# Performance work log

Hardware: AMD Instinct MI355X
Metric: run time of the kernel (lower is better)

The kernel has to match this reference:

```python
import jax, jax.numpy as jnp
import numpy as np

B, CIN, COUT, N, T, K = 16, 32, 64, 1024, 64, 3


def setup_inputs() -> dict:
    key = jax.random.key(0)
    k1, k2, k3 = jax.random.split(key, 3)
    x = jax.random.normal(k1, (B, CIN, N, T), dtype=jnp.float32)
    # scaled laplacian-like support (keep spectral radius ~1 so Chebyshev terms stay bounded)
    adj = jax.random.normal(k2, (N, N), dtype=jnp.float32) / np.sqrt(N).astype(np.float32)
    W = jax.random.normal(k3, (4 * COUT, (CIN + COUT) * K), dtype=jnp.float32) * 0.02
    b = jnp.zeros((4 * COUT,), dtype=jnp.float32)
    return {"x": x, "adj": adj, "W": W, "b": b}


def reference(x, adj, W, b):
    Bn, cin, Nn, Tn = x.shape
    c_out = W.shape[0] // 4
    feat_in = W.shape[1] // K  # = cin + c_out

    # Chebyshev polynomial basis of adj (loop-invariant across time; compute once)
    Ls = [jnp.eye(Nn, dtype=x.dtype), adj]
    for _ in range(2, K):
        Ls.append(2.0 * (adj @ Ls[-1]) - Ls[-2])
    Lap = jnp.stack(Ls, 0)  # [K, N, N]; Ls[k][q, n]

    # Conv1d(kernel=1) weight reshaped to match channel flatten order (c major, k minor)
    Wr = W.reshape(4 * c_out, feat_in, K)  # [4*c_out, F, K]
    bb = b[None, :, None]

    def step(carry, xt):
        h, c = carry
        tem = jnp.concatenate([xt, h], axis=1)  # [B, F, N]
        # einsum('bcn,knq->bckq', x, Lap.T) == einsum('bfn,kqn->bfkq', x, Lap)
        g = jnp.einsum('bfn,kqn->bfkq', tem, Lap)  # [B, F, K, N]
        fea = jnp.einsum('bfkq,ofk->boq', g, Wr) + bb  # [B, 4*c_out, N]
        i, j, f, o = jnp.split(fea, 4, axis=1)
        new_c = c * jax.nn.sigmoid(f) + jax.nn.sigmoid(i) * jnp.tanh(j)
        new_h = jnp.tanh(new_c) * jax.nn.sigmoid(o)
        return (new_h, new_c), new_h

    h0 = jnp.zeros((Bn, c_out, Nn), dtype=x.dtype)
    c0 = jnp.zeros((Bn, c_out, Nn), dtype=x.dtype)
    x_t = jnp.moveaxis(x, -1, 0)  # [T, B, cin, N]
    _, outs = jax.lax.scan(step, (h0, c0), x_t)  # [T, B, c_out, N]
    return jnp.moveaxis(outs, 0, -1)  # [B, c_out, N, T]
```

## Files before the change

### kernel.cpp

```cpp
#include <hip/hip_runtime.h>
#include <stdint.h>


#define Bb   16
#define CIN  32
#define COUT 64
#define Nn   1024
#define Tt   64
#define Ff   96
#define G4   256
#define KJ   288

#define BUFSZ 40960
#define GQPB  624
#define GQLO  19968
#define SCP   100

typedef unsigned short u16;
typedef short short8 __attribute__((ext_vector_type(8)));
typedef short short4v __attribute__((ext_vector_type(4)));
typedef float f32x4 __attribute__((ext_vector_type(4)));

static __device__ __forceinline__ u16 f2bf(float f) {
    union { float f; uint32_t u; } v; v.f = f;
    uint32_t r = v.u + 0x7FFFu + ((v.u >> 16) & 1u);
    return (u16)(r >> 16);
}
static __device__ __forceinline__ float bf2f(u16 h) {
    union { uint32_t u; float f; } v; v.u = ((uint32_t)h) << 16;
    return v.f;
}
static __device__ __forceinline__ float sigm(float x) { return 1.0f / (1.0f + expf(-x)); }

static __device__ __forceinline__ void gload16(const void* g, void* l) {
    __builtin_amdgcn_global_load_lds(
        (const __attribute__((address_space(1))) void*)g,
        (__attribute__((address_space(3))) void*)l, 16, 0, 0);
}

__global__ void k_fill(float* out, int n, float v) {
    int i = blockIdx.x * 256 + threadIdx.x;
    if (i < n) out[i] = v;
}

__global__ __launch_bounds__(256) void k_adj_split(const float* __restrict__ adj,
                                                   u16* __restrict__ hi, u16* __restrict__ lo) {
    int i = blockIdx.x * 256 + threadIdx.x;
    float v = adj[i];
    u16 h = f2bf(v);
    hi[i] = h; lo[i] = f2bf(v - bf2f(h));
}

__global__ __launch_bounds__(256) void k_adj_t(const float* __restrict__ adj,
                                               u16* __restrict__ th, u16* __restrict__ tl_) {
    __shared__ float tile[64][65];
    int m0 = blockIdx.x * 64, n0 = blockIdx.y * 64;
    int tid = threadIdx.x;
    #pragma unroll
    for (int i = 0; i < 16; i++) {
        int lin = i * 256 + tid;
        int ml = lin >> 6, nl = lin & 63;
        tile[ml][nl] = adj[(size_t)(m0 + ml) * Nn + n0 + nl];
    }
    __syncthreads();
    #pragma unroll
    for (int i = 0; i < 16; i++) {
        int lin = i * 256 + tid;
        int nl = lin >> 6, ml = lin & 63;
        float v = tile[ml][nl];
        u16 h = f2bf(v);
        size_t off = (size_t)(n0 + nl) * Nn + m0 + ml;
        th[off] = h; tl_[off] = f2bf(v - bf2f(h));
    }
}

__global__ __launch_bounds__(256) void k_l2(
    const u16* __restrict__ a_hi, const u16* __restrict__ a_lo,
    const u16* __restrict__ bt_hi, const u16* __restrict__ bt_lo,
    u16* __restrict__ o_hi, u16* __restrict__ o_lo)
{
    __shared__ u16 Ah[64][40], Al[64][40], Bh[64][40], Bl[64][40];
    const int tid = threadIdx.x, lane = tid & 63, w = tid >> 6;
    const int wm = (w >> 1) * 32, wn = (w & 1) * 32;
    const int r0 = blockIdx.x * 64, q0 = blockIdx.y * 64;
    const int srow = tid >> 2, scol = (tid & 3) * 8;
    const u16* arh = a_hi + (size_t)(r0 + srow) * Nn;
    const u16* arl = a_lo + (size_t)(r0 + srow) * Nn;
    const u16* brh = bt_hi + (size_t)(q0 + srow) * Nn;
    const u16* brl = bt_lo + (size_t)(q0 + srow) * Nn;

    f32x4 acc[2][2];
    #pragma unroll
    for (int i = 0; i < 2; i++)
        #pragma unroll
        for (int j = 0; j < 2; j++) acc[i][j] = (f32x4){0.f, 0.f, 0.f, 0.f};

    for (int k0 = 0; k0 < Nn; k0 += 32) {
        __syncthreads();
        *(short8*)&Ah[srow][scol] = *(const short8*)&arh[k0 + scol];
        *(short8*)&Al[srow][scol] = *(const short8*)&arl[k0 + scol];
        *(short8*)&Bh[srow][scol] = *(const short8*)&brh[k0 + scol];
        *(short8*)&Bl[srow][scol] = *(const short8*)&brl[k0 + scol];
        __syncthreads();
        const int kb = (lane >> 4) * 8;
        short8 ah[2], al[2], bh[2], bl[2];
        #pragma unroll
        for (int mi = 0; mi < 2; mi++) {
            int row = wm + mi * 16 + (lane & 15);
            ah[mi] = *(const short8*)&Ah[row][kb];
            al[mi] = *(const short8*)&Al[row][kb];
        }
        #pragma unroll
        for (int ni = 0; ni < 2; ni++) {
            int col = wn + ni * 16 + (lane & 15);
            bh[ni] = *(const short8*)&Bh[col][kb];
            bl[ni] = *(const short8*)&Bl[col][kb];
        }
        #pragma unroll
        for (int mi = 0; mi < 2; mi++)
            #pragma unroll
            for (int ni = 0; ni < 2; ni++) {
                acc[mi][ni] = __builtin_amdgcn_mfma_f32_16x16x32_bf16(ah[mi], bh[ni], acc[mi][ni], 0, 0, 0);
                acc[mi][ni] = __builtin_amdgcn_mfma_f32_16x16x32_bf16(al[mi], bh[ni], acc[mi][ni], 0, 0, 0);
                acc[mi][ni] = __builtin_amdgcn_mfma_f32_16x16x32_bf16(ah[mi], bl[ni], acc[mi][ni], 0, 0, 0);
            }
    }
    #pragma unroll
    for (int mi = 0; mi < 2; mi++)
        #pragma unroll
        for (int ni = 0; ni < 2; ni++)
            #pragma unroll
            for (int j = 0; j < 4; j++) {
                int rr = r0 + wm + mi * 16 + (lane >> 4) * 4 + j;
                int qq = q0 + wn + ni * 16 + (lane & 15);
                float v = 2.f * acc[mi][ni][j] - ((rr == qq) ? 1.f : 0.f);
                size_t off = (size_t)rr * Nn + qq;
                u16 hh = f2bf(v);
                o_hi[off] = hh; o_lo[off] = f2bf(v - bf2f(hh));
            }
}

__global__ __launch_bounds__(256) void k_w_split(const float* __restrict__ W,
                                                 u16* __restrict__ hi, u16* __restrict__ lo) {
    int idx = blockIdx.x * 256 + threadIdx.x;
    int o = idx / KJ, j = idx - o * KJ;
    int k = j / Ff, f = j - k * Ff;
    float v = W[(size_t)o * KJ + f * 3 + k];
    u16 h = f2bf(v);
    hi[idx] = h; lo[idx] = f2bf(v - bf2f(h));
}

__global__ __launch_bounds__(256) void k_x_split(const float* __restrict__ x,
        u16* __restrict__ xf_hi, u16* __restrict__ xf_lo) {
    __shared__ float tile[64][65];
    int n0 = blockIdx.x * 64;
    int bc = blockIdx.y;
    const float* src = x + (size_t)bc * Nn * Tt;
    int tid = threadIdx.x;
    #pragma unroll
    for (int i = 0; i < 16; i++) {
        int lin = i * 256 + tid;
        int nl = lin >> 6, tl = lin & 63;
        tile[nl][tl] = src[(size_t)(n0 + nl) * Tt + tl];
    }
    __syncthreads();
    int b = bc >> 5, ch = bc & 31;
    #pragma unroll
    for (int i = 0; i < 2; i++) {
        int item = i * 256 + tid;
        int tl = item >> 3, oct = item & 7;
        short8 vh, vl;
        #pragma unroll
        for (int m = 0; m < 8; m++) {
            float v = tile[oct * 8 + m][tl];
            u16 h = f2bf(v);
            vh[m] = (short)h;
            vl[m] = (short)f2bf(v - bf2f(h));
        }
        size_t off = (((size_t)tl * Bb + b) * CIN + ch) * Nn + n0 + oct * 8;
        *(short8*)&xf_hi[off] = vh;
        *(short8*)&xf_lo[off] = vl;
    }
}

__global__ __launch_bounds__(512, 4) void k_step(
    int t,
    const u16* __restrict__ xsf_hi, const u16* __restrict__ xsf_lo,
    u16* __restrict__ hf_hi, u16* __restrict__ hf_lo,
    const u16* __restrict__ bcat_hi, const u16* __restrict__ bcat_lo,
    const u16* __restrict__ Wh, const u16* __restrict__ Wl,
    const float* __restrict__ bias, float* __restrict__ cbuf,
    float* __restrict__ outbuf)
{
    __shared__ __attribute__((aligned(16))) char lds[81920];
    const int tid = threadIdx.x, lane = tid & 63, w = tid >> 6;
    const int bx = blockIdx.x;
    const int q0g = bx * 32;
    const int bb = blockIdx.y;

    const u16* srcb[5];
    #pragma unroll
    for (int i = 0; i < 5; i++) {
        int u = i * 512 + tid;
        if (u < 1536) {
            int hl = (u >= 768) ? 1 : 0;
            int r = (u - hl * 768) >> 3, c8 = u & 7;
            const u16* p;
            if (r < CIN) p = (hl ? xsf_lo : xsf_hi) + (size_t)((t * Bb + bb) * CIN + r) * Nn;
            else         p = (hl ? hf_lo  : hf_hi ) + (size_t)(bb * COUT + r - CIN) * Nn;
            srcb[i] = p + (c8 ^ (r & 7)) * 8;
        } else {
            int v = u - 1536;
            int hl = v >> 9;
            int r = (v & 511) >> 3, c8 = v & 7;
            int grow = q0g + (r & 31) + ((r >= 32) ? Nn : 0);
            srcb[i] = (hl ? bcat_lo : bcat_hi) + (size_t)grow * Nn + (c8 ^ (r & 7)) * 8;
        }
    }

    const int kg = w >> 2;
    const int wsub = w & 3;
    const int wr = wsub >> 1, wc = wsub & 1;
    const int ksw = kg * 4 + (lane >> 4);

    f32x4 acc[3][2];
    #pragma unroll
    for (int i = 0; i < 3; i++)
        #pragma unroll
        for (int j = 0; j < 2; j++) acc[i][j] = (f32x4){0.f, 0.f, 0.f, 0.f};

    u16 cxh[6], cxl[6];
    #pragma unroll
    for (int i = 0; i < 6; i++) { cxh[i] = 0; cxl[i] = 0; }
    const int capkc = bx >> 1;

    #pragma unroll
    for (int i = 0; i < 5; i++)
        gload16(srcb[i], lds + (i * 512 + tid) * 16);

    for (int kc = 0; kc < 16; kc++) {
        if (kc < 15) {
            char* nb = lds + ((kc + 1) & 1) * BUFSZ;
            const int k0 = (kc + 1) * 64;
            #pragma unroll
            for (int i = 0; i < 5; i++)
                gload16(srcb[i] + k0, nb + (i * 512 + tid) * 16);
            asm volatile("s_waitcnt vmcnt(5)" ::: "memory");
        } else {
            asm volatile("s_waitcnt vmcnt(0)" ::: "memory");
        }
        __builtin_amdgcn_s_barrier();
        const char* bo = lds + (kc & 1) * BUFSZ;
        {
            short8 ah[3], al[3], bh[2], bl[2];
            #pragma unroll
            for (int mi = 0; mi < 3; mi++) {
                int r = wr * 48 + mi * 16 + (lane & 15);
                int off = r * 128 + ((ksw ^ (r & 7)) << 4);
                ah[mi] = *(const short8*)(bo + off);
                al[mi] = *(const short8*)(bo + 12288 + off);
            }
            #pragma unroll
            for (int ni = 0; ni < 2; ni++) {
                int rb = wc * 32 + ni * 16 + (lane & 15);
                int off = 24576 + rb * 128 + ((ksw ^ (rb & 7)) << 4);
                bh[ni] = *(const short8*)(bo + off);
                bl[ni] = *(const short8*)(bo + 8192 + off);
            }
            __builtin_amdgcn_s_setprio(1);
            #pragma unroll
            for (int mi = 0; mi < 3; mi++)
                #pragma unroll
                for (int ni = 0; ni < 2; ni++) {
                    acc[mi][ni] = __builtin_amdgcn_mfma_f32_16x16x32_bf16(ah[mi], bh[ni], acc[mi][ni], 0, 0, 0);
                    acc[mi][ni] = __builtin_amdgcn_mfma_f32_16x16x32_bf16(al[mi], bh[ni], acc[mi][ni], 0, 0, 0);
                    acc[mi][ni] = __builtin_amdgcn_mfma_f32_16x16x32_bf16(ah[mi], bl[ni], acc[mi][ni], 0, 0, 0);
                }
            __builtin_amdgcn_s_setprio(0);
        }
        if (kc == capkc) {
            int q = lane & 31;
            int jg = (w << 1) | (lane >> 5);
            int lc = ((bx & 1) << 5) | q;
            int u8 = lc >> 3, byoff = (lc & 7) * 2;
            #pragma unroll
            for (int jj = 0; jj < 6; jj++) {
                int j = jg * 6 + jj;
                int off = j * 128 + (((u8) ^ (j & 7)) << 4) + byoff;
                cxh[jj] = *(const u16*)(bo + off);
                cxl[jj] = *(const u16*)(bo + 12288 + off);
            }
            asm volatile("s_waitcnt lgkmcnt(0)" ::: "memory");
            __builtin_amdgcn_sched_barrier(0);
        }
        __builtin_amdgcn_s_barrier();
    }

    {
        float* scratch = (float*)(lds + BUFSZ);
        if (kg == 0) {
            #pragma unroll
            for (int mi = 0; mi < 3; mi++)
                #pragma unroll
                for (int ni = 0; ni < 2; ni++) {
                    int c = wc * 32 + ni * 16 + (lane & 15);
                    int r0 = wr * 48 + mi * 16 + (lane >> 4) * 4;
                    *(f32x4*)&scratch[c * SCP + r0] = acc[mi][ni];
                }
        }
        __syncthreads();
        if (kg == 1) {
            #pragma unroll
            for (int mi = 0; mi < 3; mi++)
                #pragma unroll
                for (int ni = 0; ni < 2; ni++) {
                    int c = wc * 32 + ni * 16 + (lane & 15);
                    int r0 = wr * 48 + mi * 16 + (lane >> 4) * 4;
                    acc[mi][ni] += *(const f32x4*)&scratch[c * SCP + r0];
                }
        }
    }

    {
        int q = lane & 31;
        int jg = (w << 1) | (lane >> 5);
        #pragma unroll
        for (int jj = 0; jj < 6; jj++) {
            int j = jg * 6 + jj;
            *(u16*)(lds + q * GQPB + j * 2) = cxh[jj];
            *(u16*)(lds + GQLO + q * GQPB + j * 2) = cxl[jj];
        }
    }
    if (kg == 1) {
        #pragma unroll
        for (int mi = 0; mi < 3; mi++)
            #pragma unroll
            for (int ni = 0; ni < 2; ni++) {
                int c = wc * 32 + ni * 16 + (lane & 15);
                int g = c >> 5, ql = c & 31;
                int f0 = wr * 48 + mi * 16 + (lane >> 4) * 4;
                int jd = 96 + g * 96 + f0;
                short4v vh, vl;
                #pragma unroll
                for (int j = 0; j < 4; j++) {
                    float v = acc[mi][ni][j];
                    u16 hh = f2bf(v);
                    vh[j] = (short)hh;
                    vl[j] = (short)f2bf(v - bf2f(hh));
                }
                *(short4v*)(lds + ql * GQPB + jd * 2) = vh;
                *(short4v*)(lds + GQLO + ql * GQPB + jd * 2) = vl;
            }
    }
    __syncthreads();

    f32x4 a2[2][2];
    #pragma unroll
    for (int i = 0; i < 2; i++)
        #pragma unroll
        for (int j = 0; j < 2; j++) a2[i][j] = (f32x4){0.f, 0.f, 0.f, 0.f};

    const int kb8 = (lane >> 4) * 8;
    #pragma unroll
    for (int c = 0; c < 9; c++) {
        int j0 = c * 32;
        short8 wh[2], wl2[2], gh[2], gl[2];
        #pragma unroll
        for (int mi = 0; mi < 2; mi++) {
            int o = w * 32 + mi * 16 + (lane & 15);
            size_t so = (size_t)o * KJ + j0 + kb8;
            wh[mi]  = *(const short8*)&Wh[so];
            wl2[mi] = *(const short8*)&Wl[so];
        }
        #pragma unroll
        for (int ni = 0; ni < 2; ni++) {
            int q = ni * 16 + (lane & 15);
            int off = q * GQPB + (j0 + kb8) * 2;
            gh[ni] = *(const short8*)(lds + off);
            gl[ni] = *(const short8*)(lds + GQLO + off);
        }
        #pragma unroll
        for (int mi = 0; mi < 2; mi++)
            #pragma unroll
            for (int ni = 0; ni < 2; ni++) {
                a2[mi][ni] = __builtin_amdgcn_mfma_f32_16x16x32_bf16(wh[mi],  gh[ni], a2[mi][ni], 0, 0, 0);
                a2[mi][ni] = __builtin_amdgcn_mfma_f32_16x16x32_bf16(wl2[mi], gh[ni], a2[mi][ni], 0, 0, 0);
                a2[mi][ni] = __builtin_amdgcn_mfma_f32_16x16x32_bf16(wh[mi],  gl[ni], a2[mi][ni], 0, 0, 0);
            }
    }
    __syncthreads();

    {
        float* FEAf = (float*)lds;
        #pragma unroll
        for (int mi = 0; mi < 2; mi++) {
            int o0 = w * 32 + mi * 16 + (lane >> 4) * 4;
            f32x4 bv = *(const f32x4*)&bias[o0];
            #pragma unroll
            for (int ni = 0; ni < 2; ni++) {
                int q = ni * 16 + (lane & 15);
                #pragma unroll
                for (int j = 0; j < 4; j++)
                    FEAf[(o0 + j) * 33 + q] = a2[mi][ni][j] + bv[j];
            }
        }
    }
    __syncthreads();

    {
        const float* FEAf = (const float*)lds;
        int q = tid & 31, qg = q0g + q;
        int co0 = (tid >> 5) * 4;
        #pragma unroll
        for (int ii = 0; ii < 4; ii++) {
            int co = co0 + ii;
            float iv = FEAf[co * 33 + q];
            float jv = FEAf[(co + 64) * 33 + q];
            float fv = FEAf[(co + 128) * 33 + q];
            float ov = FEAf[(co + 192) * 33 + q];
            size_t cof = ((size_t)(bb * COUT + co)) * Nn + qg;
            float cc = cbuf[cof];
            float nc = cc * sigm(fv) + sigm(iv) * tanhf(jv);
            float nh = tanhf(nc) * sigm(ov);
            cbuf[cof] = nc;
            u16 hh = f2bf(nh);
            hf_hi[cof] = hh; hf_lo[cof] = f2bf(nh - bf2f(hh));
            outbuf[((size_t)(t * Bb + bb) * COUT + co) * Nn + qg] = nh;
        }
    }
}

__global__ __launch_bounds__(256) void k_out_t(const float* __restrict__ outbuf,
                                               float* __restrict__ out) {
    __shared__ float tile[64][65];
    int q0 = blockIdx.x * 64;
    int bo = blockIdx.y;
    int b = bo >> 6, o = bo & 63;
    int tid = threadIdx.x;
    #pragma unroll
    for (int i = 0; i < 16; i++) {
        int lin = i * 256 + tid;
        int tl = lin >> 6, ql = lin & 63;
        tile[tl][ql] = outbuf[(((size_t)tl * Bb + b) * COUT + o) * Nn + q0 + ql];
    }
    __syncthreads();
    #pragma unroll
    for (int i = 0; i < 16; i++) {
        int lin = i * 256 + tid;
        int ql = lin >> 6, tl = lin & 63;
        out[((size_t)bo * Nn + q0 + ql) * Tt + tl] = tile[tl][ql];
    }
}

extern "C" void kernel_launch(void* const* d_in, const int* in_sizes, int n_in,
                              void* d_out, int out_size, void* d_ws, size_t ws_size,
                              hipStream_t stream)
{
    const float* x    = (const float*)d_in[0];
    const float* adj  = (const float*)d_in[1];
    const float* W    = (const float*)d_in[2];
    const float* bias = (const float*)d_in[3];
    float* out = (float*)d_out;

    size_t off = 0;
    char* base = (char*)d_ws;
    auto take = [&](size_t bytes) -> void* {
        void* r = base + off;
        off += (bytes + 255) & ~(size_t)255;
        return r;
    };
    u16* bcat_hi = (u16*)take(2ull * 2 * Nn * Nn);
    u16* bcat_lo = (u16*)take(2ull * 2 * Nn * Nn);
    u16* adjT_hi = (u16*)take(2ull * Nn * Nn);
    u16* adjT_lo = (u16*)take(2ull * Nn * Nn);
    u16* xsf_hi  = (u16*)take(2ull * Tt * Bb * CIN * Nn);
    u16* xsf_lo  = (u16*)take(2ull * Tt * Bb * CIN * Nn);
    u16* hf_hi   = (u16*)take(2ull * Bb * COUT * Nn);
    u16* hf_lo   = (u16*)take(2ull * Bb * COUT * Nn);
    float* cbuf  = (float*)take(4ull * Bb * COUT * Nn);
    u16* Wc_hi   = (u16*)take(2ull * G4 * KJ);
    u16* Wc_lo   = (u16*)take(2ull * G4 * KJ);
    float* outbuf = (float*)take(4ull * (size_t)Tt * Bb * COUT * Nn);

    if (off > ws_size) {
        float v = (float)(ws_size >> 20);
        k_fill<<<dim3((out_size + 255) / 256), 256, 0, stream>>>(out, out_size, v);
        return;
    }

    hipMemsetAsync(hf_hi, 0, 2ull * Bb * COUT * Nn, stream);
    hipMemsetAsync(hf_lo, 0, 2ull * Bb * COUT * Nn, stream);
    hipMemsetAsync(cbuf, 0, 4ull * Bb * COUT * Nn, stream);

    k_adj_split<<<dim3((Nn * Nn) / 256), 256, 0, stream>>>(adj, bcat_hi, bcat_lo);
    k_adj_t<<<dim3(16, 16), 256, 0, stream>>>(adj, adjT_hi, adjT_lo);
    k_l2<<<dim3(16, 16), 256, 0, stream>>>(bcat_hi, bcat_lo, adjT_hi, adjT_lo,
                                           bcat_hi + (size_t)Nn * Nn, bcat_lo + (size_t)Nn * Nn);
    k_w_split<<<dim3((G4 * KJ) / 256), 256, 0, stream>>>(W, Wc_hi, Wc_lo);
    k_x_split<<<dim3(Nn / 64, Bb * CIN), 256, 0, stream>>>(x, xsf_hi, xsf_lo);

    for (int t = 0; t < Tt; t++) {
        k_step<<<dim3(32, 16), 512, 0, stream>>>(t,
            xsf_hi, xsf_lo, hf_hi, hf_lo,
            bcat_hi, bcat_lo, Wc_hi, Wc_lo,
            bias, cbuf, outbuf);
    }
    k_out_t<<<dim3(Nn / 64, Bb * COUT), 256, 0, stream>>>(outbuf, out);
}
```

Measured before the change: 2.514 ms.

## Load adjacency B fragments directly to registers and double-buffer hidden state

The Chebyshev-basis (bcat) operand is no longer staged through LDS. Each lane now reads its B fragments straight from global memory into registers, which shrinks the shared buffers from about 80KB to about 49KB and cuts the per-iteration async loads from five to three. The hidden state becomes ping-pong input/output buffers, which removes the in-place read/write hazard between blocks within a step. A `reps` loop is added, along with an extra launch that runs eight repetitions into separate scratch buffers before the real time loop. That launch adds extra kernel work on every call.

```diff
diff --git a/kernel.cpp b/kernel.cpp
--- a/kernel.cpp
+++ b/kernel.cpp
@@ -11,7 +11,7 @@
 #define G4   256
 #define KJ   288
 
-#define BUFSZ 40960
+#define ABUF  24576
 #define GQPB  624
 #define GQLO  19968
 #define SCP   100
@@ -184,249 +184,254 @@
 }
 
 __global__ __launch_bounds__(512, 4) void k_step(
-    int t,
+    int t, int reps,
     const u16* __restrict__ xsf_hi, const u16* __restrict__ xsf_lo,
-    u16* __restrict__ hf_hi, u16* __restrict__ hf_lo,
+    const u16* __restrict__ hin_hi, const u16* __restrict__ hin_lo,
+    u16* __restrict__ hout_hi, u16* __restrict__ hout_lo,
     const u16* __restrict__ bcat_hi, const u16* __restrict__ bcat_lo,
     const u16* __restrict__ Wh, const u16* __restrict__ Wl,
     const float* __restrict__ bias, float* __restrict__ cbuf,
     float* __restrict__ outbuf)
 {
-    __shared__ __attribute__((aligned(16))) char lds[81920];
+    __shared__ __attribute__((aligned(16))) char lds[50176];
     const int tid = threadIdx.x, lane = tid & 63, w = tid >> 6;
     const int bx = blockIdx.x;
     const int q0g = bx * 32;
     const int bb = blockIdx.y;
 
-    const u16* srcb[5];
-    #pragma unroll
-    for (int i = 0; i < 5; i++) {
+    const u16* srcb[3];
+    #pragma unroll
+    for (int i = 0; i < 3; i++) {
         int u = i * 512 + tid;
-        if (u < 1536) {
-            int hl = (u >= 768) ? 1 : 0;
-            int r = (u - hl * 768) >> 3, c8 = u & 7;
-            const u16* p;
-            if (r < CIN) p = (hl ? xsf_lo : xsf_hi) + (size_t)((t * Bb + bb) * CIN + r) * Nn;
-            else         p = (hl ? hf_lo  : hf_hi ) + (size_t)(bb * COUT + r - CIN) * Nn;
-            srcb[i] = p + (c8 ^ (r & 7)) * 8;
-        } else {
-            int v = u - 1536;
-            int hl = v >> 9;
-            int r = (v & 511) >> 3, c8 = v & 7;
-            int grow = q0g + (r & 31) + ((r >= 32) ? Nn : 0);
-            srcb[i] = (hl ? bcat_lo : bcat_hi) + (size_t)grow * Nn + (c8 ^ (r & 7)) * 8;
-        }
+        int hl = (u >= 768) ? 1 : 0;
+        int r = (u - hl * 768) >> 3, c8 = u & 7;
+        const u16* p;
+        if (r < CIN) p = (hl ? xsf_lo : xsf_hi) + (size_t)((t * Bb + bb) * CIN + r) * Nn;
+        else         p = (hl ? hin_lo : hin_hi) + (size_t)(bb * COUT + r - CIN) * Nn;
+        srcb[i] = p + (c8 ^ (r & 7)) * 8;
     }
 
     const int kg = w >> 2;
     const int wsub = w & 3;
     const int wr = wsub >> 1, wc = wsub & 1;
     const int ksw = kg * 4 + (lane >> 4);
-
-    f32x4 acc[3][2];
-    #pragma unroll
-    for (int i = 0; i < 3; i++)
-        #pragma unroll
-        for (int j = 0; j < 2; j++) acc[i][j] = (f32x4){0.f, 0.f, 0.f, 0.f};
-
-    u16 cxh[6], cxl[6];
-    #pragma unroll
-    for (int i = 0; i < 6; i++) { cxh[i] = 0; cxl[i] = 0; }
     const int capkc = bx >> 1;
 
-    #pragma unroll
-    for (int i = 0; i < 5; i++)
-        gload16(srcb[i], lds + (i * 512 + tid) * 16);
-
-    for (int kc = 0; kc < 16; kc++) {
-        if (kc < 15) {
-            char* nb = lds + ((kc + 1) & 1) * BUFSZ;
-            const int k0 = (kc + 1) * 64;
-            #pragma unroll
-            for (int i = 0; i < 5; i++)
-                gload16(srcb[i] + k0, nb + (i * 512 + tid) * 16);
-            asm volatile("s_waitcnt vmcnt(5)" ::: "memory");
-        } else {
-            asm volatile("s_waitcnt vmcnt(0)" ::: "memory");
-        }
-        __builtin_amdgcn_s_barrier();
-        const char* bo = lds + (kc & 1) * BUFSZ;
+    const u16 *bp_h[2], *bp_l[2];
+    #pragma unroll
+    for (int ni = 0; ni < 2; ni++) {
+        int rb = wc * 32 + ni * 16 + (lane & 15);
+        int grow = q0g + (rb & 31) + ((rb >= 32) ? Nn : 0);
+        bp_h[ni] = bcat_hi + (size_t)grow * Nn + ksw * 8;
+        bp_l[ni] = bcat_lo + (size_t)grow * Nn + ksw * 8;
+    }
+
+    for (int rep = 0; rep < reps; rep++) {
+        f32x4 acc[3][2];
+        #pragma unroll
+        for (int i = 0; i < 3; i++)
+            #pragma unroll
+            for (int j = 0; j < 2; j++) acc[i][j] = (f32x4){0.f, 0.f, 0.f, 0.f};
+
+        u16 cxh[6], cxl[6];
+        #pragma unroll
+        for (int i = 0; i < 6; i++) { cxh[i] = 0; cxl[i] = 0; }
+
+        #pragma unroll
+        for (int i = 0; i < 3; i++)
+            gload16(srcb[i], lds + (i * 512 + tid) * 16);
+
+        for (int kc = 0; kc < 16; kc++) {
+            short8 bh[2], bl[2];
+            #pragma unroll
+            for (int ni = 0; ni < 2; ni++) {
+                bh[ni] = *(const short8*)&bp_h[ni][kc * 64];
+                bl[ni] = *(const short8*)&bp_l[ni][kc * 64];
+            }
+            if (kc < 15) {
+                char* nb = lds + ((kc + 1) & 1) * ABUF;
+                const int k0 = (kc + 1) * 64;
+                #pragma unroll
+                for (int i = 0; i < 3; i++)
+                    gload16(srcb[i] + k0, nb + (i * 512 + tid) * 16);
+                asm volatile("s_waitcnt vmcnt(7)" ::: "memory");
+            } else {
+                asm volatile("s_waitcnt vmcnt(4)" ::: "memory");
+            }
+            __builtin_amdgcn_s_barrier();
+            const char* bo = lds + (kc & 1) * ABUF;
+            {
+                short8 ah[3], al[3];
+                #pragma unroll
+                for (int mi = 0; mi < 3; mi++) {
+                    int r = wr * 48 + mi * 16 + (lane & 15);
+                    int off = r * 128 + ((ksw ^ (r & 7)) << 4);
+                    ah[mi] = *(const short8*)(bo + off);
+                    al[mi] = *(const short8*)(bo + 12288 + off);
+                }
+                __builtin_amdgcn_s_setprio(1);
+                #pragma unroll
+                for (int mi = 0; mi < 3; mi++)
+                    #pragma unroll
+                    for (int ni = 0; ni < 2; ni++) {
+                        acc[mi][ni] = __builtin_amdgcn_mfma_f32_16x16x32_bf16(ah[mi], bh[ni], acc[mi][ni], 0, 0, 0);
+                        acc[mi][ni] = __builtin_amdgcn_mfma_f32_16x16x32_bf16(al[mi], bh[ni], acc[mi][ni], 0, 0, 0);
+                        acc[mi][ni] = __builtin_amdgcn_mfma_f32_16x16x32_bf16(ah[mi], bl[ni], acc[mi][ni], 0, 0, 0);
+                    }
+                __builtin_amdgcn_s_setprio(0);
+            }
+            if (kc == capkc) {
+                int q = lane & 31;
+                int jg = (w << 1) | (lane >> 5);
+                int lc = ((bx & 1) << 5) | q;
+                int u8 = lc >> 3, byoff = (lc & 7) * 2;
+                #pragma unroll
+                for (int jj = 0; jj < 6; jj++) {
+                    int j = jg * 6 + jj;
+                    int off = j * 128 + (((u8) ^ (j & 7)) << 4) + byoff;
+                    cxh[jj] = *(const u16*)(bo + off);
+                    cxl[jj] = *(const u16*)(bo + 12288 + off);
+                }
+                asm volatile("s_waitcnt lgkmcnt(0)" ::: "memory");
+                __builtin_amdgcn_sched_barrier(0);
+            }
+            __builtin_amdgcn_s_barrier();
+        }
+
         {
-            short8 ah[3], al[3], bh[2], bl[2];
-            #pragma unroll
-            for (int mi = 0; mi < 3; mi++) {
-                int r = wr * 48 + mi * 16 + (lane & 15);
-                int off = r * 128 + ((ksw ^ (r & 7)) << 4);
-                ah[mi] = *(const short8*)(bo + off);
-                al[mi] = *(const short8*)(bo + 12288 + off);
-            }
-            #pragma unroll
-            for (int ni = 0; ni < 2; ni++) {
-                int rb = wc * 32 + ni * 16 + (lane & 15);
-                int off = 24576 + rb * 128 + ((ksw ^ (rb & 7)) << 4);
-                bh[ni] = *(const short8*)(bo + off);
-                bl[ni] = *(const short8*)(bo + 8192 + off);
-            }
-            __builtin_amdgcn_s_setprio(1);
-            #pragma unroll
-            for (int mi = 0; mi < 3; mi++)
-                #pragma unroll
-                for (int ni = 0; ni < 2; ni++) {
-                    acc[mi][ni] = __builtin_amdgcn_mfma_f32_16x16x32_bf16(ah[mi], bh[ni], acc[mi][ni], 0, 0, 0);
-                    acc[mi][ni] = __builtin_amdgcn_mfma_f32_16x16x32_bf16(al[mi], bh[ni], acc[mi][ni], 0, 0, 0);
-                    acc[mi][ni] = __builtin_amdgcn_mfma_f32_16x16x32_bf16(ah[mi], bl[ni], acc[mi][ni], 0, 0, 0);
-                }
-            __builtin_amdgcn_s_setprio(0);
-        }
-        if (kc == capkc) {
+            float* scratch = (float*)(lds + ABUF);
+            if (kg == 0) {
+                #pragma unroll
+                for (int mi = 0; mi < 3; mi++)
+                    #pragma unroll
+                    for (int ni = 0; ni < 2; ni++) {
+                        int c = wc * 32 + ni * 16 + (lane & 15);
+                        int r0 = wr * 48 + mi * 16 + (lane >> 4) * 4;
+                        *(f32x4*)&scratch[c * SCP + r0] = acc[mi][ni];
+                    }
+            }
+            __syncthreads();
+            if (kg == 1) {
+                #pragma unroll
+                for (int mi = 0; mi < 3; mi++)
+                    #pragma unroll
+                    for (int ni = 0; ni < 2; ni++) {
+                        int c = wc * 32 + ni * 16 + (lane & 15);
+                        int r0 = wr * 48 + mi * 16 + (lane >> 4) * 4;
+                        acc[mi][ni] += *(const f32x4*)&scratch[c * SCP + r0];
+                    }
+            }
+            __syncthreads();
+        }
+
+        {
             int q = lane & 31;
             int jg = (w << 1) | (lane >> 5);
-            int lc = ((bx & 1) << 5) | q;
-            int u8 = lc >> 3, byoff = (lc & 7) * 2;
             #pragma unroll
             for (int jj = 0; jj < 6; jj++) {
                 int j = jg * 6 + jj;
-                int off = j * 128 + (((u8) ^ (j & 7)) << 4) + byoff;
-                cxh[jj] = *(const u16*)(bo + off);
-                cxl[jj] = *(const u16*)(bo + 12288 + off);
-            }
-            asm volatile("s_waitcnt lgkmcnt(0)" ::: "memory");
-            __builtin_amdgcn_sched_barrier(0);
-        }
-        __builtin_amdgcn_s_barrier();
-    }
-
-    {
-        float* scratch = (float*)(lds + BUFSZ);
-        if (kg == 0) {
+                *(u16*)(lds + q * GQPB + j * 2) = cxh[jj];
+                *(u16*)(lds + GQLO + q * GQPB + j * 2) = cxl[jj];
+            }
+        }
+        if (kg == 1) {
             #pragma unroll
             for (int mi = 0; mi < 3; mi++)
                 #pragma unroll
                 for (int ni = 0; ni < 2; ni++) {
                     int c = wc * 32 + ni * 16 + (lane & 15);
-                    int r0 = wr * 48 + mi * 16 + (lane >> 4) * 4;
-                    *(f32x4*)&scratch[c * SCP + r0] = acc[mi][ni];
+                    int g = c >> 5, ql = c & 31;
+                    int f0 = wr * 48 + mi * 16 + (lane >> 4) * 4;
+                    int jd = 96 + g * 96 + f0;
+                    short4v vh, vl;
+                    #pragma unroll
+                    for (int j = 0; j < 4; j++) {
+                        float v = acc[mi][ni][j];
+                        u16 hh = f2bf(v);
+                        vh[j] = (short)hh;
+                        vl[j] = (short)f2bf(v - bf2f(hh));
+                    }
+                    *(short4v*)(lds + ql * GQPB + jd * 2) = vh;
+                    *(short4v*)(lds + GQLO + ql * GQPB + jd * 2) = vl;
                 }
         }
         __syncthreads();
-        if (kg == 1) {
-            #pragma unroll
-            for (int mi = 0; mi < 3; mi++)
-                #pragma unroll
-                for (int ni = 0; ni < 2; ni++) {
-                    int c = wc * 32 + ni * 16 + (lane & 15);
-                    int r0 = wr * 48 + mi * 16 + (lane >> 4) * 4;
-                    acc[mi][ni] += *(const f32x4*)&scratch[c * SCP + r0];
-                }
-        }
-    }
-
-    {
-        int q = lane & 31;
-        int jg = (w << 1) | (lane >> 5);
-        #pragma unroll
-        for (int jj = 0; jj < 6; jj++) {
-            int j = jg * 6 + jj;
-            *(u16*)(lds + q * GQPB + j * 2) = cxh[jj];
-            *(u16*)(lds + GQLO + q * GQPB + j * 2) = cxl[jj];
-        }
-    }
-    if (kg == 1) {
-        #pragma unroll
-        for (int mi = 0; mi < 3; mi++)
-            #pragma unroll
-            for (int ni = 0; ni < 2; ni++) {
-                int c = wc * 32 + ni * 16 + (lane & 15);
-                int g = c >> 5, ql = c & 31;
-                int f0 = wr * 48 + mi * 16 + (lane >> 4) * 4;
-                int jd = 96 + g * 96 + f0;
-                short4v vh, vl;
-                #pragma unroll
-                for (int j = 0; j < 4; j++) {
-                    float v = acc[mi][ni][j];
-                    u16 hh = f2bf(v);
-                    vh[j] = (short)hh;
-                    vl[j] = (short)f2bf(v - bf2f(hh));
-                }
-                *(short4v*)(lds + ql * GQPB + jd * 2) = vh;
-                *(short4v*)(lds + GQLO + ql * GQPB + jd * 2) = vl;
-            }
-    }
-    __syncthreads();
-
-    f32x4 a2[2][2];
-    #pragma unroll
-    for (int i = 0; i < 2; i++)
-        #pragma unroll
-        for (int j = 0; j < 2; j++) a2[i][j] = (f32x4){0.f, 0.f, 0.f, 0.f};
-
-    const int kb8 = (lane >> 4) * 8;
-    #pragma unroll
-    for (int c = 0; c < 9; c++) {
-        int j0 = c * 32;
-        short8 wh[2], wl2[2], gh[2], gl[2];
-        #pragma unroll
-        for (int mi = 0; mi < 2; mi++) {
-            int o = w * 32 + mi * 16 + (lane & 15);
-            size_t so = (size_t)o * KJ + j0 + kb8;
-            wh[mi]  = *(const short8*)&Wh[so];
-            wl2[mi] = *(const short8*)&Wl[so];
-        }
-        #pragma unroll
-        for (int ni = 0; ni < 2; ni++) {
-            int q = ni * 16 + (lane & 15);
-            int off = q * GQPB + (j0 + kb8) * 2;
-            gh[ni] = *(const short8*)(lds + off);
-            gl[ni] = *(const short8*)(lds + GQLO + off);
-        }
-        #pragma unroll
-        for (int mi = 0; mi < 2; mi++)
-            #pragma unroll
-            for (int ni = 0; ni < 2; ni++) {
-                a2[mi][ni] = __builtin_amdgcn_mfma_f32_16x16x32_bf16(wh[mi],  gh[ni], a2[mi][ni], 0, 0, 0);
-                a2[mi][ni] = __builtin_amdgcn_mfma_f32_16x16x32_bf16(wl2[mi], gh[ni], a2[mi][ni], 0, 0, 0);
-                a2[mi][ni] = __builtin_amdgcn_mfma_f32_16x16x32_bf16(wh[mi],  gl[ni], a2[mi][ni], 0, 0, 0);
-            }
-    }
-    __syncthreads();
-
-    {
-        float* FEAf = (float*)lds;
-        #pragma unroll
-        for (int mi = 0; mi < 2; mi++) {
-            int o0 = w * 32 + mi * 16 + (lane >> 4) * 4;
-            f32x4 bv = *(const f32x4*)&bias[o0];
+
+        f32x4 a2[2][2];
+        #pragma unroll
+        for (int i = 0; i < 2; i++)
+            #pragma unroll
+            for (int j = 0; j < 2; j++) a2[i][j] = (f32x4){0.f, 0.f, 0.f, 0.f};
+
+        const int kb8 = (lane >> 4) * 8;
+        #pragma unroll
+        for (int c = 0; c < 9; c++) {
+            int j0 = c * 32;
+            short8 wh[2], wl2[2], gh[2], gl[2];
+            #pragma unroll
+            for (int mi = 0; mi < 2; mi++) {
+                int o = w * 32 + mi * 16 + (lane & 15);
+                size_t so = (size_t)o * KJ + j0 + kb8;
+                wh[mi]  = *(const short8*)&Wh[so];
+                wl2[mi] = *(const short8*)&Wl[so];
+            }
             #pragma unroll
             for (int ni = 0; ni < 2; ni++) {
                 int q = ni * 16 + (lane & 15);
-                #pragma unroll
-                for (int j = 0; j < 4; j++)
-                    FEAf[(o0 + j) * 33 + q] = a2[mi][ni][j] + bv[j];
-            }
-        }
-    }
-    __syncthreads();
-
-    {
-        const float* FEAf = (const float*)lds;
-        int q = tid & 31, qg = q0g + q;
-        int co0 = (tid >> 5) * 4;
-        #pragma unroll
-        for (int ii = 0; ii < 4; ii++) {
-            int co = co0 + ii;
-            float iv = FEAf[co * 33 + q];
-            float jv = FEAf[(co + 64) * 33 + q];
-            float fv = FEAf[(co + 128) * 33 + q];
-            float ov = FEAf[(co + 192) * 33 + q];
-            size_t cof = ((size_t)(bb * COUT + co)) * Nn + qg;
-            float cc = cbuf[cof];
-            float nc = cc * sigm(fv) + sigm(iv) * tanhf(jv);
-            float nh = tanhf(nc) * sigm(ov);
-            cbuf[cof] = nc;
-            u16 hh = f2bf(nh);
-            hf_hi[cof] = hh; hf_lo[cof] = f2bf(nh - bf2f(hh));
-            outbuf[((size_t)(t * Bb + bb) * COUT + co) * Nn + qg] = nh;
-        }
+                int off = q * GQPB + (j0 + kb8) * 2;
+                gh[ni] = *(const short8*)(lds + off);
+                gl[ni] = *(const short8*)(lds + GQLO + off);
+            }
+            #pragma unroll
+            for (int mi = 0; mi < 2; mi++)
+                #pragma unroll
+                for (int ni = 0; ni < 2; ni++) {
+                    a2[mi][ni] = __builtin_amdgcn_mfma_f32_16x16x32_bf16(wh[mi],  gh[ni], a2[mi][ni], 0, 0, 0);
+                    a2[mi][ni] = __builtin_amdgcn_mfma_f32_16x16x32_bf16(wl2[mi], gh[ni], a2[mi][ni], 0, 0, 0);
+                    a2[mi][ni] = __builtin_amdgcn_mfma_f32_16x16x32_bf16(wh[mi],  gl[ni], a2[mi][ni], 0, 0, 0);
+                }
+        }
+        __syncthreads();
+
+        {
+            float* FEAf = (float*)lds;
+            #pragma unroll
+            for (int mi = 0; mi < 2; mi++) {
+                int o0 = w * 32 + mi * 16 + (lane >> 4) * 4;
+                f32x4 bv = *(const f32x4*)&bias[o0];
+                #pragma unroll
+                for (int ni = 0; ni < 2; ni++) {
+                    int q = ni * 16 + (lane & 15);
+                    #pragma unroll
+                    for (int j = 0; j < 4; j++)
+                        FEAf[(o0 + j) * 33 + q] = a2[mi][ni][j] + bv[j];
+                }
+            }
+        }
+        __syncthreads();
+
+        {
+            const float* FEAf = (const float*)lds;
+            int q = tid & 31, qg = q0g + q;
+            int co0 = (tid >> 5) * 4;
+            #pragma unroll
+            for (int ii = 0; ii < 4; ii++) {
+                int co = co0 + ii;
+                float iv = FEAf[co * 33 + q];
+                float jv = FEAf[(co + 64) * 33 + q];
+                float fv = FEAf[(co + 128) * 33 + q];
+                float ov = FEAf[(co + 192) * 33 + q];
+                size_t cof = ((size_t)(bb * COUT + co)) * Nn + qg;
+                float cc = cbuf[cof];
+                float nc = cc * sigm(fv) + sigm(iv) * tanhf(jv);
+                float nh = tanhf(nc) * sigm(ov);
+                cbuf[cof] = nc;
+                u16 hh = f2bf(nh);
+                hout_hi[cof] = hh; hout_lo[cof] = f2bf(nh - bf2f(hh));
+                outbuf[((size_t)(t * Bb + bb) * COUT + co) * Nn + qg] = nh;
+            }
+        }
+        if (rep != reps - 1) __syncthreads();
     }
 }
 
@@ -475,12 +480,18 @@
     u16* adjT_lo = (u16*)take(2ull * Nn * Nn);
     u16* xsf_hi  = (u16*)take(2ull * Tt * Bb * CIN * Nn);
     u16* xsf_lo  = (u16*)take(2ull * Tt * Bb * CIN * Nn);
-    u16* hf_hi   = (u16*)take(2ull * Bb * COUT * Nn);
-    u16* hf_lo   = (u16*)take(2ull * Bb * COUT * Nn);
+    u16* hfA_hi  = (u16*)take(2ull * Bb * COUT * Nn);
+    u16* hfA_lo  = (u16*)take(2ull * Bb * COUT * Nn);
+    u16* hfB_hi  = (u16*)take(2ull * Bb * COUT * Nn);
+    u16* hfB_lo  = (u16*)take(2ull * Bb * COUT * Nn);
     float* cbuf  = (float*)take(4ull * Bb * COUT * Nn);
     u16* Wc_hi   = (u16*)take(2ull * G4 * KJ);
     u16* Wc_lo   = (u16*)take(2ull * G4 * KJ);
     float* outbuf = (float*)take(4ull * (size_t)Tt * Bb * COUT * Nn);
+    u16* prH_hi  = (u16*)take(2ull * Bb * COUT * Nn);
+    u16* prH_lo  = (u16*)take(2ull * Bb * COUT * Nn);
+    float* prC   = (float*)take(4ull * Bb * COUT * Nn);
+    float* prOut = (float*)take(4ull * Bb * COUT * Nn);
 
     if (off > ws_size) {
         float v = (float)(ws_size >> 20);
@@ -488,9 +499,10 @@
         return;
     }
 
-    hipMemsetAsync(hf_hi, 0, 2ull * Bb * COUT * Nn, stream);
-    hipMemsetAsync(hf_lo, 0, 2ull * Bb * COUT * Nn, stream);
+    hipMemsetAsync(hfA_hi, 0, 2ull * Bb * COUT * Nn, stream);
+    hipMemsetAsync(hfA_lo, 0, 2ull * Bb * COUT * Nn, stream);
     hipMemsetAsync(cbuf, 0, 4ull * Bb * COUT * Nn, stream);
+    hipMemsetAsync(prC,  0, 4ull * Bb * COUT * Nn, stream);
 
     k_adj_split<<<dim3((Nn * Nn) / 256), 256, 0, stream>>>(adj, bcat_hi, bcat_lo);
     k_adj_t<<<dim3(16, 16), 256, 0, stream>>>(adj, adjT_hi, adjT_lo);
@@ -499,11 +511,18 @@
     k_w_split<<<dim3((G4 * KJ) / 256), 256, 0, stream>>>(W, Wc_hi, Wc_lo);
     k_x_split<<<dim3(Nn / 64, Bb * CIN), 256, 0, stream>>>(x, xsf_hi, xsf_lo);
 
+    k_step<<<dim3(32, 16), 512, 0, stream>>>(0, 8,
+        xsf_hi, xsf_lo, hfA_hi, hfA_lo, prH_hi, prH_lo,
+        bcat_hi, bcat_lo, Wc_hi, Wc_lo, bias, prC, prOut);
+
     for (int t = 0; t < Tt; t++) {
-        k_step<<<dim3(32, 16), 512, 0, stream>>>(t,
-            xsf_hi, xsf_lo, hf_hi, hf_lo,
-            bcat_hi, bcat_lo, Wc_hi, Wc_lo,
-            bias, cbuf, outbuf);
+        const u16* hi_in  = (t & 1) ? hfB_hi : hfA_hi;
+        const u16* lo_in  = (t & 1) ? hfB_lo : hfA_lo;
+        u16* hi_out = (t & 1) ? hfA_hi : hfB_hi;
+        u16* lo_out = (t & 1) ? hfA_lo : hfB_lo;
+        k_step<<<dim3(32, 16), 512, 0, stream>>>(t, 1,
+            xsf_hi, xsf_lo, hi_in, lo_in, hi_out, lo_out,
+            bcat_hi, bcat_lo, Wc_hi, Wc_lo, bias, cbuf, outbuf);
     }
     k_out_t<<<dim3(Nn / 64, Bb * COUT), 256, 0, stream>>>(outbuf, out);
 }
```

Measured after the change: 9.043 ms. 260% more time.
